# Kernel tuning notes

Hardware: AMD Instinct MI355X
Metric: run time of the kernel (lower is better)

Reference implementation:

```python
import jax, jax.numpy as jnp
import numpy as np

RADIUS = 3  # local window half-size -> K = (2*RADIUS+1)**2 = 49 taps


def _bilinear_sample_zeros(img_flat, x, y, h, w):
    """Bilinear sampling with zeros padding (grid_sample, align_corners=True).
    img_flat: (B, C, H*W); x, y: (P, K) pixel-space coords. Returns (B, C, P, K).
    align_corners=True denormalization exactly inverts the normalization in the
    original module, so we sample directly at pixel coordinates.
    """
    B, C, _ = img_flat.shape
    x0 = jnp.floor(x)
    y0 = jnp.floor(y)
    out = jnp.zeros((B, C) + x.shape, dtype=img_flat.dtype)
    corners = [
        (x0,       y0,       (x0 + 1 - x) * (y0 + 1 - y)),
        (x0 + 1.0, y0,       (x - x0) * (y0 + 1 - y)),
        (x0,       y0 + 1.0, (x0 + 1 - x) * (y - y0)),
        (x0 + 1.0, y0 + 1.0, (x - x0) * (y - y0)),
    ]
    for xi, yi, wt in corners:
        inb = (xi >= 0) & (xi < w) & (yi >= 0) & (yi < h)
        xi_c = jnp.clip(xi, 0, w - 1).astype(jnp.int32)
        yi_c = jnp.clip(yi, 0, h - 1).astype(jnp.int32)
        idx = (yi_c * w + xi_c).reshape(-1)            # (P*K,)
        v = jnp.take(img_flat, idx, axis=2)            # (B, C, P*K)
        v = v.reshape(B, C, *x.shape)                  # (B, C, P, K)
        out = out + v * (wt * inb.astype(img_flat.dtype))[None, None]
    return out


def reference(feature0, feature1):
    n, c, s, h, w = feature0.shape
    B = n * s
    f0 = feature0.transpose(0, 2, 1, 3, 4).reshape(B, c, h, w)
    f1 = feature1.transpose(0, 2, 1, 3, 4).reshape(B, c, h, w)

    r = RADIUS
    # base pixel coords (x, y), flattened row-major over (h, w) -> (P, 2)
    yy, xx = jnp.meshgrid(jnp.arange(h, dtype=jnp.float32),
                          jnp.arange(w, dtype=jnp.float32), indexing='ij')
    base = jnp.stack([xx, yy], axis=-1).reshape(h * w, 2)  # (P, 2)

    # window offsets (dx, dy), dy outer / dx inner ordering -> (K, 2)
    dys, dxs = jnp.meshgrid(jnp.arange(-r, r + 1, dtype=jnp.float32),
                            jnp.arange(-r, r + 1, dtype=jnp.float32), indexing='ij')
    offs = jnp.stack([dxs, dys], axis=-1).reshape(-1, 2)   # (K, 2)

    sample = base[:, None, :] + offs[None, :, :]           # (P, K, 2)
    valid = ((sample[..., 0] >= 0) & (sample[..., 0] < w) &
             (sample[..., 1] >= 0) & (sample[..., 1] < h))  # (P, K)

    f1_flat = f1.reshape(B, c, h * w)
    wf = _bilinear_sample_zeros(f1_flat, sample[..., 0], sample[..., 1], h, w)  # (B, c, P, K)

    f0_flat = f0.reshape(B, c, h * w)
    corr = jnp.einsum('bcp,bcpk->bpk', f0_flat, wf) / jnp.asarray(c, jnp.float32) ** 0.5
    corr = jnp.where(valid[None], corr, -jnp.inf)
    prob = jax.nn.softmax(corr, axis=-1)                   # (B, P, K)

    corresp = jnp.einsum('bpk,pkj->bpj', prob, sample)     # (B, P, 2) expected (x, y)
    flow = corresp - base[None]                            # (B, P, 2)
    flow = flow.reshape(n, s, h, w, 2).transpose(0, 4, 1, 2, 3)  # (n, 2, s, h, w)
    return flow


def setup_inputs() -> dict:
    key = jax.random.key(0)
    k0, k1 = jax.random.split(key)
    n, c, s, h, w = 2, 64, 4, 64, 44
    feature0 = jax.random.normal(k0, (n, c, s, h, w), dtype=jnp.float32)
    feature1 = jax.random.normal(k1, (n, c, s, h, w), dtype=jnp.float32)
    return {"feature0": feature0, "feature1": feature1}
```

## Files before the change

### kernel.cpp

```cpp
#include <hip/hip_runtime.h>
#include <math.h>

#define N_  2
#define C_  64
#define S_  4
#define H_  64
#define W_  44
#define HW_       (H_ * W_)
#define CH_STRIDE (S_ * HW_)
#define NSTRIDE   (C_ * S_ * HW_)

typedef _Float16 h8 __attribute__((ext_vector_type(8)));
typedef float    f4 __attribute__((ext_vector_type(4)));

__global__ __launch_bounds__(512) void flow_kernel(
    const float* __restrict__ f0,
    const float* __restrict__ f1,
    float* __restrict__ out)
{
    const int lane = threadIdx.x & 63;
    const int w    = threadIdx.x >> 6;

    const int b = blockIdx.x & 7;
    const int y = blockIdx.x >> 3;
    const int n_idx = b >> 2;
    const int s_idx = b & 3;
    const int base  = n_idx * NSTRIDE + s_idx * HW_;

    __shared__ __align__(16) _Float16 slabF1[7 * 8 * 64 * 8];
    __shared__ __align__(16) _Float16 slabF0[8 * 48 * 8];
    __shared__ float corr[W_][49];

    const int row     = y + w - 3;
    const bool row_ok = (row >= 0) && (row < H_);

    if (w < 7) {
        if (row_ok) {
            const int col   = lane - 8;
            const bool vld  = (col >= 0) && (col < W_);
            const int cc    = min(max(col, 0), W_ - 1);
            const float* p  = f1 + base + row * W_ + cc;
            float v[64];
            #pragma unroll
            for (int j = 0; j < 64; ++j)
                v[j] = p[(size_t)j * CH_STRIDE];
            #pragma unroll
            for (int c8 = 0; c8 < 8; ++c8) {
                h8 pk;
                #pragma unroll
                for (int j = 0; j < 8; ++j)
                    pk[j] = vld ? (_Float16)v[c8 * 8 + j] : (_Float16)0.0f;
                *(h8*)&slabF1[((w * 8 + c8) * 64 + lane) * 8] = pk;
            }
        }
    } else {
        if (lane < 48) {
            const bool vld = (lane < W_);
            const int  xc  = min(lane, W_ - 1);
            const float* p = f0 + base + y * W_ + xc;
            float v[64];
            #pragma unroll
            for (int j = 0; j < 64; ++j)
                v[j] = p[(size_t)j * CH_STRIDE];
            #pragma unroll
            for (int c8 = 0; c8 < 8; ++c8) {
                h8 pk;
                #pragma unroll
                for (int j = 0; j < 8; ++j)
                    pk[j] = vld ? (_Float16)v[c8 * 8 + j] : (_Float16)0.0f;
                *(h8*)&slabF0[(c8 * 48 + lane) * 8] = pk;
            }
        }
    }

    __syncthreads();

    if (w < 7 && row_ok) {
        const int quad = lane >> 4;
        const int l16  = lane & 15;

        h8 afr[3][2];
        #pragma unroll
        for (int mi = 0; mi < 3; ++mi)
            #pragma unroll
            for (int kh = 0; kh < 2; ++kh)
                afr[mi][kh] = *(const h8*)
                    &slabF0[((kh * 4 + quad) * 48 + (mi * 16 + l16)) * 8];

        const _Float16* myslab = &slabF1[w * (8 * 64 * 8)];
        f4 acc[3][2];
        #pragma unroll
        for (int mi = 0; mi < 3; ++mi) {
            #pragma unroll
            for (int nh = 0; nh < 2; ++nh) {
                f4 a = {0.f, 0.f, 0.f, 0.f};
                #pragma unroll
                for (int kh = 0; kh < 2; ++kh) {
                    const h8 bfr = *(const h8*)
                        &myslab[((kh * 4 + quad) * 64 + (mi * 16 + nh * 16 + l16)) * 8];
                    a = __builtin_amdgcn_mfma_f32_16x16x32_f16(afr[mi][kh], bfr, a, 0, 0, 0);
                }
                acc[mi][nh] = a;
            }
        }

        #pragma unroll
        for (int mi = 0; mi < 3; ++mi) {
            #pragma unroll
            for (int nh = 0; nh < 2; ++nh) {
                #pragma unroll
                for (int r = 0; r < 4; ++r) {
                    const int x   = mi * 16 + quad * 4 + r;
                    const int col = mi * 16 + nh * 16 - 8 + l16;
                    const int dx  = col - x + 3;
                    if (x < W_ && dx >= 0 && dx < 7)
                        corr[x][w * 7 + dx] = acc[mi][nh][r] * 0.125f;
                }
            }
        }
    }

    __syncthreads();

    if (w == 0) {
        const int xe = min(lane, W_ - 1);
        float c[49];
        float m = -1e30f;
        #pragma unroll
        for (int k = 0; k < 49; ++k) {
            const int kdy = k / 7, kdx = k % 7;
            const int col = lane + kdx - 3;
            const int rr  = y + kdy - 3;
            const bool ok = (col >= 0) && (col < W_) && (rr >= 0) && (rr < H_);
            const float v = ok ? corr[xe][k] : -1e30f;
            c[k] = v;
            m = fmaxf(m, v);
        }
        float S = 0.0f, Sx = 0.0f, Sy = 0.0f;
        #pragma unroll
        for (int k = 0; k < 49; ++k) {
            const float e = __expf(c[k] - m);
            S  += e;
            Sx += e * (float)(k % 7 - 3);
            Sy += e * (float)(k / 7 - 3);
        }
        if (lane < W_) {
            const float inv = 1.0f / S;
            const int ob = (n_idx * 2) * S_ * HW_ + s_idx * HW_ + y * W_ + lane;
            out[ob]            = Sx * inv;
            out[ob + S_ * HW_] = Sy * inv;
        }
    }
}

extern "C" void kernel_launch(void* const* d_in, const int* in_sizes, int n_in,
                              void* d_out, int out_size, void* d_ws, size_t ws_size,
                              hipStream_t stream) {
    const float* f0 = (const float*)d_in[0];
    const float* f1 = (const float*)d_in[1];
    float* out = (float*)d_out;

    flow_kernel<<<8 * H_, 512, 0, stream>>>(f0, f1, out);
}
```

Before: 66.00 us.

## Split fp32-to-fp16 packing into a separate pre-pass kernel via workspace

Adds a pack kernel that converts each input row once into an fp16 channel-blocked layout in workspace. The flow kernel then loads MFMA fragments straight from global memory instead of staging slabs in LDS. This removes the seven-fold redundant strided fp32 loads of each f1 row across neighbouring blocks, and the per-block register-heavy transposition. The cost is a second kernel launch and an extra global write and read of the packed data.

```diff
diff --git a/kernel.cpp b/kernel.cpp
--- a/kernel.cpp
+++ b/kernel.cpp
@@ -13,9 +13,53 @@
 typedef _Float16 h8 __attribute__((ext_vector_type(8)));
 typedef float    f4 __attribute__((ext_vector_type(4)));
 
-__global__ __launch_bounds__(512) void flow_kernel(
+#define PF1_ELEMS (8 * 8 * 64 * 64 * 8)
+
+__global__ __launch_bounds__(512) void pack_kernel(
     const float* __restrict__ f0,
     const float* __restrict__ f1,
+    _Float16* __restrict__ pf1,
+    _Float16* __restrict__ pf0)
+{
+    const int lane = threadIdx.x & 63;
+    const int c8   = threadIdx.x >> 6;
+    const int b    = blockIdx.x & 7;
+    const int row  = blockIdx.x >> 3;
+    const int n_idx = b >> 2;
+    const int s_idx = b & 3;
+    const int base  = n_idx * NSTRIDE + s_idx * HW_ + row * W_
+                    + c8 * 8 * CH_STRIDE;
+
+    {
+        const int  col = lane - 8;
+        const bool vld = (col >= 0) && (col < W_);
+        const int  cc  = min(max(col, 0), W_ - 1);
+        const float* p = f1 + base + cc;
+        float v[8];
+        #pragma unroll
+        for (int j = 0; j < 8; ++j) v[j] = p[(size_t)j * CH_STRIDE];
+        h8 pk;
+        #pragma unroll
+        for (int j = 0; j < 8; ++j) pk[j] = vld ? (_Float16)v[j] : (_Float16)0.0f;
+        *(h8*)&pf1[((((b * 8 + c8) * 64) + row) * 64 + lane) * 8] = pk;
+    }
+    if (lane < 48) {
+        const bool vld = (lane < W_);
+        const int  xc  = min(lane, W_ - 1);
+        const float* p = f0 + base + xc;
+        float v[8];
+        #pragma unroll
+        for (int j = 0; j < 8; ++j) v[j] = p[(size_t)j * CH_STRIDE];
+        h8 pk;
+        #pragma unroll
+        for (int j = 0; j < 8; ++j) pk[j] = vld ? (_Float16)v[j] : (_Float16)0.0f;
+        *(h8*)&pf0[((((b * 8 + c8) * 64) + row) * 48 + lane) * 8] = pk;
+    }
+}
+
+__global__ __launch_bounds__(448) void flow_kernel(
+    const _Float16* __restrict__ pf1,
+    const _Float16* __restrict__ pf0,
     float* __restrict__ out)
 {
     const int lane = threadIdx.x & 63;
@@ -25,69 +69,25 @@
     const int y = blockIdx.x >> 3;
     const int n_idx = b >> 2;
     const int s_idx = b & 3;
-    const int base  = n_idx * NSTRIDE + s_idx * HW_;
 
-    __shared__ __align__(16) _Float16 slabF1[7 * 8 * 64 * 8];
-    __shared__ __align__(16) _Float16 slabF0[8 * 48 * 8];
     __shared__ float corr[W_][49];
 
     const int row     = y + w - 3;
     const bool row_ok = (row >= 0) && (row < H_);
 
-    if (w < 7) {
-        if (row_ok) {
-            const int col   = lane - 8;
-            const bool vld  = (col >= 0) && (col < W_);
-            const int cc    = min(max(col, 0), W_ - 1);
-            const float* p  = f1 + base + row * W_ + cc;
-            float v[64];
-            #pragma unroll
-            for (int j = 0; j < 64; ++j)
-                v[j] = p[(size_t)j * CH_STRIDE];
-            #pragma unroll
-            for (int c8 = 0; c8 < 8; ++c8) {
-                h8 pk;
-                #pragma unroll
-                for (int j = 0; j < 8; ++j)
-                    pk[j] = vld ? (_Float16)v[c8 * 8 + j] : (_Float16)0.0f;
-                *(h8*)&slabF1[((w * 8 + c8) * 64 + lane) * 8] = pk;
-            }
-        }
-    } else {
-        if (lane < 48) {
-            const bool vld = (lane < W_);
-            const int  xc  = min(lane, W_ - 1);
-            const float* p = f0 + base + y * W_ + xc;
-            float v[64];
-            #pragma unroll
-            for (int j = 0; j < 64; ++j)
-                v[j] = p[(size_t)j * CH_STRIDE];
-            #pragma unroll
-            for (int c8 = 0; c8 < 8; ++c8) {
-                h8 pk;
-                #pragma unroll
-                for (int j = 0; j < 8; ++j)
-                    pk[j] = vld ? (_Float16)v[c8 * 8 + j] : (_Float16)0.0f;
-                *(h8*)&slabF0[(c8 * 48 + lane) * 8] = pk;
-            }
-        }
-    }
+    const int quad = lane >> 4;
+    const int l16  = lane & 15;
 
-    __syncthreads();
-
-    if (w < 7 && row_ok) {
-        const int quad = lane >> 4;
-        const int l16  = lane & 15;
-
+    if (row_ok) {
         h8 afr[3][2];
         #pragma unroll
         for (int mi = 0; mi < 3; ++mi)
             #pragma unroll
             for (int kh = 0; kh < 2; ++kh)
                 afr[mi][kh] = *(const h8*)
-                    &slabF0[((kh * 4 + quad) * 48 + (mi * 16 + l16)) * 8];
+                    &pf0[((((b * 8 + (kh * 4 + quad)) * 64) + y) * 48
+                          + (mi * 16 + l16)) * 8];
 
-        const _Float16* myslab = &slabF1[w * (8 * 64 * 8)];
         f4 acc[3][2];
         #pragma unroll
         for (int mi = 0; mi < 3; ++mi) {
@@ -97,7 +97,8 @@
                 #pragma unroll
                 for (int kh = 0; kh < 2; ++kh) {
                     const h8 bfr = *(const h8*)
-                        &myslab[((kh * 4 + quad) * 64 + (mi * 16 + nh * 16 + l16)) * 8];
+                        &pf1[((((b * 8 + (kh * 4 + quad)) * 64) + row) * 64
+                              + (mi * 16 + nh * 16 + l16)) * 8];
                     a = __builtin_amdgcn_mfma_f32_16x16x32_f16(afr[mi][kh], bfr, a, 0, 0, 0);
                 }
                 acc[mi][nh] = a;
@@ -159,6 +160,9 @@
     const float* f0 = (const float*)d_in[0];
     const float* f1 = (const float*)d_in[1];
     float* out = (float*)d_out;
+    _Float16* pf1 = (_Float16*)d_ws;
+    _Float16* pf0 = pf1 + PF1_ELEMS;
 
-    flow_kernel<<<8 * H_, 512, 0, stream>>>(f0, f1, out);
+    pack_kernel<<<8 * H_, 512, 0, stream>>>(f0, f1, pf1, pf0);
+    flow_kernel<<<8 * H_, 448, 0, stream>>>(pf1, pf0, out);
 }
```

New measurement: 68.62 us. 4.0% more time.
